# Performance work log

Measured on AMD Instinct MI355X. Metric: run time of the kernel, lower is better.

Reference implementation:

```python
import jax, jax.numpy as jnp
import numpy as np

M = 0.25      # margin m
GAMMA = 64.0  # scale gamma
N, D = 8192, 128
NUM_CLASSES = 512


def setup_inputs() -> dict:
    key = jax.random.key(0)
    k1, k2 = jax.random.split(key)
    inputs = jax.random.normal(k1, (N, D), dtype=jnp.float32)
    targets = jax.random.randint(k2, (N,), 0, NUM_CLASSES, dtype=jnp.int64)
    return {"inputs": inputs, "targets": targets}


def reference(inputs, targets):
    # L2-normalize rows -> cosine similarity matrix [n, n]
    x = inputs / jnp.linalg.norm(inputs, axis=1, keepdims=True)
    sim = x @ x.T
    # positive mask: same label (includes diagonal, matching the torch code)
    mask = targets[:, None] == targets[None, :]

    Op, On = 1.0 + M, -M
    delta_p, delta_n = 1.0 - M, M

    sim_d = jax.lax.stop_gradient(sim)  # .detach() in torch
    ap = jnp.maximum(Op - sim_d, 0.0)
    an = jnp.maximum(sim_d + On, 0.0)

    logit_p = -ap * (sim - delta_p) * GAMMA
    logit_n = an * (sim - delta_n) * GAMMA

    neg_inf = jnp.float32(-jnp.inf)
    # per-row logsumexp over positives of -logit_p, over negatives of logit_n
    lp = jax.nn.logsumexp(jnp.where(mask, -logit_p, neg_inf), axis=1)
    ln = jax.nn.logsumexp(jnp.where(mask, neg_inf, logit_n), axis=1)

    return jnp.mean(jax.nn.softplus(ln + lp))
```

## Files before the change

kernel.cpp:

```cpp
#include <hip/hip_runtime.h>
#include <math.h>


#define NR    8192
#define DIMK  128
#define NT    64
#define CHUNK 4
#define NBLKS 544

typedef __attribute__((ext_vector_type(8))) short short8;
typedef __attribute__((ext_vector_type(4))) float f32x4;
typedef __attribute__((address_space(3))) uint32_t lds_u32;
typedef const __attribute__((address_space(1))) uint32_t glb_u32;

__device__ __forceinline__ unsigned short bf16_rne(float f) {
  uint32_t u = __float_as_uint(f);
  u += 0x7FFFu + ((u >> 16) & 1u);
  return (unsigned short)(u >> 16);
}


__global__ __launch_bounds__(256) void normalize_split_kernel(
    const float* __restrict__ x, unsigned short* __restrict__ xhi,
    unsigned short* __restrict__ xlo, float* __restrict__ gP,
    float* __restrict__ gN, int* __restrict__ counter) {
  if (blockIdx.x < 32)      gP[blockIdx.x * 256 + threadIdx.x] = 0.f;
  else if (blockIdx.x < 64) gN[(blockIdx.x - 32) * 256 + threadIdx.x] = 0.f;
  if (blockIdx.x == 64 && threadIdx.x == 0) *counter = 0;

  const int wave = threadIdx.x >> 6;
  const int lane = threadIdx.x & 63;
  const int row  = blockIdx.x * 4 + wave;
  const float2 v = ((const float2*)(x + (size_t)row * DIMK))[lane];
  float ss = v.x * v.x + v.y * v.y;
  #pragma unroll
  for (int s = 1; s < 64; s <<= 1) ss += __shfl_xor(ss, s);
  const float r = rsqrtf(ss);
  const float a = v.x * r, b = v.y * r;
  const unsigned short ha = bf16_rne(a), hb = bf16_rne(b);
  const float haf = __uint_as_float((uint32_t)ha << 16);
  const float hbf = __uint_as_float((uint32_t)hb << 16);
  ushort2 hi, lo;
  hi.x = ha; hi.y = hb;
  lo.x = bf16_rne(a - haf); lo.y = bf16_rne(b - hbf);
  ((ushort2*)xhi)[(size_t)row * 64 + lane] = hi;
  ((ushort2*)xlo)[(size_t)row * 64 + lane] = lo;
}

__global__ __launch_bounds__(512, 2) void simloss_kernel(
    const unsigned short* __restrict__ xhi, const unsigned short* __restrict__ xlo,
    const int* __restrict__ tgt, float* __restrict__ gP, float* __restrict__ gN,
    int* __restrict__ counter, float* __restrict__ out) {
  __shared__ unsigned short S[32768];
  __shared__ int tAs[128];
  __shared__ int tBs[2][128];
  __shared__ float red[512];
  __shared__ int islast;

  const int tid  = threadIdx.x;
  const int wave = tid >> 6, lane = tid & 63;
  const int wy = wave & 3, wx = wave >> 2;
  const int q = lane >> 4, mcol = lane & 15;

  int w = blockIdx.x, bi = 0, sz = NT;
  while (w >= (sz + CHUNK - 1) / CHUNK) { w -= (sz + CHUNK - 1) / CHUNK; ++bi; --sz; }
  const int bj0 = bi + w * CHUNK;
  const int ntile = min(CHUNK, NT - bj0);
  const int i0 = bi * 128;

  {
    const unsigned short* ghA = xhi + (size_t)i0 * DIMK;
    const unsigned short* glA = xlo + (size_t)i0 * DIMK;
    #pragma unroll
    for (int g = 0; g < 4; ++g) {
      const int r  = wave * 16 + g * 4 + (lane >> 4);
      const int sc = (lane & 15) ^ (r & 15);
      __builtin_amdgcn_global_load_lds((glb_u32*)(ghA + (size_t)r * DIMK + sc * 8),
          (lds_u32*)&S[(wave * 16 + g * 4) * 128], 16, 0, 0);
      __builtin_amdgcn_global_load_lds((glb_u32*)(glA + (size_t)r * DIMK + sc * 8),
          (lds_u32*)&S[16384 + (wave * 16 + g * 4) * 128], 16, 0, 0);
    }
  }
  if (tid < 128) tAs[tid] = tgt[i0 + tid];
  __syncthreads();

  short8 Ah[2][4], Al[2][4];
  #pragma unroll
  for (int fr = 0; fr < 2; ++fr) {
    const int r = wy * 32 + fr * 16 + mcol;
    #pragma unroll
    for (int ks = 0; ks < 4; ++ks) {
      const int pc = (ks * 4 + q) ^ mcol;
      Ah[fr][ks] = *(const short8*)&S[r * 128 + pc * 8];
      Al[fr][ks] = *(const short8*)&S[16384 + r * 128 + pc * 8];
    }
  }
  int ta[2][4];
  #pragma unroll
  for (int fr = 0; fr < 2; ++fr)
    #pragma unroll
    for (int rg = 0; rg < 4; ++rg)
      ta[fr][rg] = tAs[wy * 32 + fr * 16 + q * 4 + rg];
  __builtin_amdgcn_s_waitcnt(0);
  __syncthreads();

  if (tid < 128) tBs[0][tid] = tgt[bj0 * 128 + tid];
  {
    const unsigned short* gb = xhi + (size_t)bj0 * 128 * DIMK;
    #pragma unroll
    for (int g = 0; g < 4; ++g) {
      const int r  = wave * 16 + g * 4 + (lane >> 4);
      const int sc = (lane & 15) ^ (r & 15);
      __builtin_amdgcn_global_load_lds((glb_u32*)(gb + (size_t)r * DIMK + sc * 8),
          (lds_u32*)&S[(wave * 16 + g * 4) * 128], 16, 0, 0);
    }
  }

  float rowP[2][4] = {{0.f}}, rowN[2][4] = {{0.f}};
  float pP[4], pN[4];
  int pcol = -1;

  for (int t = 0; t < ntile; ++t) {
    const int bj = bj0 + t;
    __builtin_amdgcn_s_waitcnt(112);
    __builtin_amdgcn_s_barrier();

    if (t + 1 < ntile) {
      if (tid < 128) tBs[(t + 1) & 1][tid] = tgt[(bj + 1) * 128 + tid];
      const unsigned short* gb = xhi + (size_t)(bj + 1) * 128 * DIMK;
      unsigned short* dst = &S[((t + 1) & 1) * 16384];
      #pragma unroll
      for (int g = 0; g < 4; ++g) {
        const int r  = wave * 16 + g * 4 + (lane >> 4);
        const int sc = (lane & 15) ^ (r & 15);
        __builtin_amdgcn_global_load_lds((glb_u32*)(gb + (size_t)r * DIMK + sc * 8),
            (lds_u32*)&dst[(wave * 16 + g * 4) * 128], 16, 0, 0);
      }
    }

    const unsigned short* Bb = &S[(t & 1) * 16384];
    f32x4 acc[2][4];
    #pragma unroll
    for (int fr = 0; fr < 2; ++fr)
      #pragma unroll
      for (int fc = 0; fc < 4; ++fc)
        acc[fr][fc] = (f32x4){0.f, 0.f, 0.f, 0.f};
    #pragma unroll
    for (int ks = 0; ks < 4; ++ks) {
      short8 bh[4];
      #pragma unroll
      for (int fc = 0; fc < 4; ++fc) {
        const int rb = wx * 64 + fc * 16 + mcol;
        const int pc = (ks * 4 + q) ^ mcol;
        bh[fc] = *(const short8*)&Bb[rb * 128 + pc * 8];
      }
      #pragma unroll
      for (int fc = 0; fc < 4; ++fc) {
        acc[0][fc] = __builtin_amdgcn_mfma_f32_16x16x32_bf16(Ah[0][ks], bh[fc], acc[0][fc], 0, 0, 0);
        acc[1][fc] = __builtin_amdgcn_mfma_f32_16x16x32_bf16(Ah[1][ks], bh[fc], acc[1][fc], 0, 0, 0);
        acc[0][fc] = __builtin_amdgcn_mfma_f32_16x16x32_bf16(Al[0][ks], bh[fc], acc[0][fc], 0, 0, 0);
        acc[1][fc] = __builtin_amdgcn_mfma_f32_16x16x32_bf16(Al[1][ks], bh[fc], acc[1][fc], 0, 0, 0);
      }
    }

    if (pcol >= 0) {
      #pragma unroll
      for (int fc = 0; fc < 4; ++fc) {
        float a = pP[fc], b = pN[fc];
        a += __shfl_xor(a, 16); a += __shfl_xor(a, 32);
        b += __shfl_xor(b, 16); b += __shfl_xor(b, 32);
        if (q == 0) {
          atomicAdd(&gP[pcol + fc * 16 + mcol], a);
          atomicAdd(&gN[pcol + fc * 16 + mcol], b);
        }
      }
    }

    int tb[4];
    #pragma unroll
    for (int fc = 0; fc < 4; ++fc) tb[fc] = tBs[t & 1][wx * 64 + fc * 16 + mcol];
    float cP[4] = {0.f, 0.f, 0.f, 0.f}, cN[4] = {0.f, 0.f, 0.f, 0.f};
    #pragma unroll
    for (int fr = 0; fr < 2; ++fr) {
      #pragma unroll
      for (int rg = 0; rg < 4; ++rg) {
        const int taa = ta[fr][rg];
        float vp = 0.f, vn = 0.f;
        #pragma unroll
        for (int fc = 0; fc < 4; ++fc) {
          const float s  = acc[fr][fc][rg];
          const bool pos = (taa == tb[fc]);
          const float ap = fmaxf(1.25f - s, 0.f);
          const float an = fmaxf(s - 0.25f, 0.f);
          const float arg = pos ? ap * fmaf(s, 64.f, -48.f) : an * an * 64.f;
          const float e = __expf(arg);
          const float ep = pos ? e : 0.f;
          const float en = pos ? 0.f : e;
          vp += ep; vn += en;
          cP[fc] += ep; cN[fc] += en;
        }
        rowP[fr][rg] += vp;
        rowN[fr][rg] += vn;
      }
    }
    if (bj != bi) {
      #pragma unroll
      for (int fc = 0; fc < 4; ++fc) { pP[fc] = cP[fc]; pN[fc] = cN[fc]; }
      pcol = bj * 128 + wx * 64;
    } else {
      pcol = -1;
    }
  }

  if (pcol >= 0) {
    #pragma unroll
    for (int fc = 0; fc < 4; ++fc) {
      float a = pP[fc], b = pN[fc];
      a += __shfl_xor(a, 16); a += __shfl_xor(a, 32);
      b += __shfl_xor(b, 16); b += __shfl_xor(b, 32);
      if (q == 0) {
        atomicAdd(&gP[pcol + fc * 16 + mcol], a);
        atomicAdd(&gN[pcol + fc * 16 + mcol], b);
      }
    }
  }

  #pragma unroll
  for (int fr = 0; fr < 2; ++fr) {
    #pragma unroll
    for (int rg = 0; rg < 4; ++rg) {
      float vp = rowP[fr][rg], vn = rowN[fr][rg];
      #pragma unroll
      for (int m = 1; m < 16; m <<= 1) {
        vp += __shfl_xor(vp, m);
        vn += __shfl_xor(vn, m);
      }
      if (mcol == 0) {
        const int row = i0 + wy * 32 + fr * 16 + q * 4 + rg;
        atomicAdd(&gP[row], vp);
        atomicAdd(&gN[row], vn);
      }
    }
  }

  __builtin_amdgcn_s_waitcnt(0);
  __syncthreads();
  if (tid == 0) islast = (atomicAdd(counter, 1) == NBLKS - 1) ? 1 : 0;
  __syncthreads();
  if (islast) {
    float local = 0.f;
    #pragma unroll 1
    for (int b = 0; b < 2; ++b) {
      const int base = b * 4096 + tid * 8;
      float p[8], n[8];
      #pragma unroll
      for (int u = 0; u < 8; ++u) p[u] = atomicAdd(&gP[base + u], 0.0f);
      #pragma unroll
      for (int u = 0; u < 8; ++u) n[u] = atomicAdd(&gN[base + u], 0.0f);
      #pragma unroll
      for (int u = 0; u < 8; ++u) local += log1pf(p[u] * n[u]);
    }
    red[tid] = local;
    __syncthreads();
    for (int s2 = 256; s2 > 0; s2 >>= 1) {
      if (tid < s2) red[tid] += red[tid + s2];
      __syncthreads();
    }
    if (tid == 0) out[0] = red[0] / (float)NR;
  }
}

extern "C" void kernel_launch(void* const* d_in, const int* in_sizes, int n_in,
                              void* d_out, int out_size, void* d_ws, size_t ws_size,
                              hipStream_t stream) {
  const float* x  = (const float*)d_in[0];
  const int* tgt  = (const int*)d_in[1];
  float* out      = (float*)d_out;

  unsigned short* xhi = (unsigned short*)d_ws;
  unsigned short* xlo = xhi + (size_t)NR * DIMK;
  float* gP = (float*)((char*)d_ws + (size_t)NR * DIMK * 4);
  float* gN = gP + NR;
  int* counter = (int*)(gN + NR);

  normalize_split_kernel<<<NR / 4, 256, 0, stream>>>(x, xhi, xlo, gP, gN, counter);
  simloss_kernel<<<NBLKS, 512, 0, stream>>>(xhi, xlo, tgt, gP, gN, counter, out);
}
```

Measured before the change: 130.8 us.

## Balance triangular tile work with paired row-strips and LDS column reduction

Replaces the chunked upper-triangle tile schedule (544 blocks with uneven tile counts) with a paired-strip scheme: strip p and strip 63-p are concatenated into 65 tiles split evenly across 16 blocks, so each of the 512 blocks gets 4-5 tiles. Column partial sums are now reduced across waves through an LDS buffer and written by a single wave, instead of every wave issuing atomics. B-tile staging is restricted to four of the waves, and the launch bound is raised to 4 blocks per CU. This adds extra barriers per tile and an A-strip reload at the strip switch, and the larger LDS footprint may keep the occupancy hint from being met.

```diff
diff --git a/kernel.cpp b/kernel.cpp
--- a/kernel.cpp
+++ b/kernel.cpp
@@ -5,8 +5,7 @@
 #define NR    8192
 #define DIMK  128
 #define NT    64
-#define CHUNK 4
-#define NBLKS 544
+#define NBLKS 512
 
 typedef __attribute__((ext_vector_type(8))) short short8;
 typedef __attribute__((ext_vector_type(4))) float f32x4;
@@ -47,13 +46,14 @@
   ((ushort2*)xlo)[(size_t)row * 64 + lane] = lo;
 }
 
-__global__ __launch_bounds__(512, 2) void simloss_kernel(
+__global__ __launch_bounds__(512, 4) void simloss_kernel(
     const unsigned short* __restrict__ xhi, const unsigned short* __restrict__ xlo,
     const int* __restrict__ tgt, float* __restrict__ gP, float* __restrict__ gN,
     int* __restrict__ counter, float* __restrict__ out) {
   __shared__ unsigned short S[32768];
-  __shared__ int tAs[128];
-  __shared__ int tBs[2][128];
+  __shared__ float colbuf[2][4][128][2];
+  __shared__ int tAs[2][128];
+  __shared__ int tBs[5][128];
   __shared__ float red[512];
   __shared__ int islast;
 
@@ -61,84 +61,132 @@
   const int wave = tid >> 6, lane = tid & 63;
   const int wy = wave & 3, wx = wave >> 2;
   const int q = lane >> 4, mcol = lane & 15;
-
-  int w = blockIdx.x, bi = 0, sz = NT;
-  while (w >= (sz + CHUNK - 1) / CHUNK) { w -= (sz + CHUNK - 1) / CHUNK; ++bi; --sz; }
-  const int bj0 = bi + w * CHUNK;
-  const int ntile = min(CHUNK, NT - bj0);
-  const int i0 = bi * 128;
-
-  {
-    const unsigned short* ghA = xhi + (size_t)i0 * DIMK;
-    const unsigned short* glA = xlo + (size_t)i0 * DIMK;
+  const bool isStage = (wy == 1) || (wy == 2);
+  const bool isFlush = (wy == 0);
+  const int srank = (wy - 1) + wx * 2;
+
+  const int p  = blockIdx.x >> 4;
+  const int b  = blockIdx.x & 15;
+  const int n1 = NT - p;
+  const int t0 = (b * (NT + 1)) >> 4;
+  const int t1 = ((b + 1) * (NT + 1)) >> 4;
+  const int ntile = t1 - t0;
+  const int p2 = NT - 1 - p;
+
+  int cur_bi = (t0 < n1) ? p : p2;
+
+  if (tid < 128)       tAs[0][tid] = tgt[cur_bi * 128 + tid];
+  else if (tid < 256)  tAs[1][tid - 128] = tgt[p2 * 128 + (tid - 128)];
+  for (int v = tid; v < ntile * 128; v += 512) {
+    const int ix = t0 + (v >> 7);
+    const int bj = (ix < n1) ? p + ix : p2 + (ix - n1);
+    tBs[v >> 7][v & 127] = tgt[bj * 128 + (v & 127)];
+  }
+
+  auto stageA = [&](int bi) {
+    const unsigned short* gh = xhi + (size_t)bi * 128 * DIMK;
+    const unsigned short* gl = xlo + (size_t)bi * 128 * DIMK;
     #pragma unroll
     for (int g = 0; g < 4; ++g) {
       const int r  = wave * 16 + g * 4 + (lane >> 4);
       const int sc = (lane & 15) ^ (r & 15);
-      __builtin_amdgcn_global_load_lds((glb_u32*)(ghA + (size_t)r * DIMK + sc * 8),
+      __builtin_amdgcn_global_load_lds((glb_u32*)(gh + (size_t)r * DIMK + sc * 8),
           (lds_u32*)&S[(wave * 16 + g * 4) * 128], 16, 0, 0);
-      __builtin_amdgcn_global_load_lds((glb_u32*)(glA + (size_t)r * DIMK + sc * 8),
+      __builtin_amdgcn_global_load_lds((glb_u32*)(gl + (size_t)r * DIMK + sc * 8),
           (lds_u32*)&S[16384 + (wave * 16 + g * 4) * 128], 16, 0, 0);
     }
-  }
-  if (tid < 128) tAs[tid] = tgt[i0 + tid];
-  __syncthreads();
-
-  short8 Ah[2][4], Al[2][4];
-  #pragma unroll
-  for (int fr = 0; fr < 2; ++fr) {
-    const int r = wy * 32 + fr * 16 + mcol;
-    #pragma unroll
-    for (int ks = 0; ks < 4; ++ks) {
-      const int pc = (ks * 4 + q) ^ mcol;
-      Ah[fr][ks] = *(const short8*)&S[r * 128 + pc * 8];
-      Al[fr][ks] = *(const short8*)&S[16384 + r * 128 + pc * 8];
-    }
-  }
-  int ta[2][4];
-  #pragma unroll
-  for (int fr = 0; fr < 2; ++fr)
-    #pragma unroll
-    for (int rg = 0; rg < 4; ++rg)
-      ta[fr][rg] = tAs[wy * 32 + fr * 16 + q * 4 + rg];
-  __builtin_amdgcn_s_waitcnt(0);
-  __syncthreads();
-
-  if (tid < 128) tBs[0][tid] = tgt[bj0 * 128 + tid];
-  {
-    const unsigned short* gb = xhi + (size_t)bj0 * 128 * DIMK;
-    #pragma unroll
-    for (int g = 0; g < 4; ++g) {
-      const int r  = wave * 16 + g * 4 + (lane >> 4);
+  };
+  auto stageB = [&](int bj, int buf) {
+    const unsigned short* gb = xhi + (size_t)bj * 128 * DIMK;
+    unsigned short* dst = &S[buf * 16384];
+    #pragma unroll
+    for (int g = 0; g < 8; ++g) {
+      const int r  = srank * 32 + g * 4 + (lane >> 4);
       const int sc = (lane & 15) ^ (r & 15);
       __builtin_amdgcn_global_load_lds((glb_u32*)(gb + (size_t)r * DIMK + sc * 8),
-          (lds_u32*)&S[(wave * 16 + g * 4) * 128], 16, 0, 0);
-    }
-  }
+          (lds_u32*)&dst[(srank * 32 + g * 4) * 128], 16, 0, 0);
+    }
+  };
+
+  short8 Ah[2][4], Al[2][4];
+  int ta[2][4];
+  auto extractA = [&](int seg) {
+    #pragma unroll
+    for (int fr = 0; fr < 2; ++fr) {
+      const int r = wy * 32 + fr * 16 + mcol;
+      #pragma unroll
+      for (int ks = 0; ks < 4; ++ks) {
+        const int pc = (ks * 4 + q) ^ mcol;
+        Ah[fr][ks] = *(const short8*)&S[r * 128 + pc * 8];
+        Al[fr][ks] = *(const short8*)&S[16384 + r * 128 + pc * 8];
+      }
+    }
+    #pragma unroll
+    for (int fr = 0; fr < 2; ++fr)
+      #pragma unroll
+      for (int rg = 0; rg < 4; ++rg)
+        ta[fr][rg] = tAs[seg][wy * 32 + fr * 16 + q * 4 + rg];
+  };
 
   float rowP[2][4] = {{0.f}}, rowN[2][4] = {{0.f}};
-  float pP[4], pN[4];
-  int pcol = -1;
-
-  for (int t = 0; t < ntile; ++t) {
-    const int bj = bj0 + t;
-    __builtin_amdgcn_s_waitcnt(112);
+  auto flushRows = [&](int bi) {
+    #pragma unroll
+    for (int fr = 0; fr < 2; ++fr)
+      #pragma unroll
+      for (int rg = 0; rg < 4; ++rg) {
+        float vp = rowP[fr][rg], vn = rowN[fr][rg];
+        #pragma unroll
+        for (int m = 1; m < 16; m <<= 1) {
+          vp += __shfl_xor(vp, m);
+          vn += __shfl_xor(vn, m);
+        }
+        if (mcol == 0) {
+          const int row = bi * 128 + wy * 32 + fr * 16 + q * 4 + rg;
+          atomicAdd(&gP[row], vp);
+          atomicAdd(&gN[row], vn);
+        }
+      }
+  };
+
+  stageA(cur_bi);
+  __syncthreads();
+  extractA(0);
+  __builtin_amdgcn_s_waitcnt(49279);
+  __builtin_amdgcn_s_barrier();
+  if (isStage) stageB((t0 < n1) ? p + t0 : p2 + (t0 - n1), 0);
+
+  for (int tl = 0; tl < ntile; ++tl) {
+    const int ix = t0 + tl;
+    const int bi = (ix < n1) ? p : p2;
+    const int bj = (ix < n1) ? p + ix : p2 + (ix - n1);
+
+    if (bi != cur_bi) {
+      flushRows(cur_bi);
+      cur_bi = bi;
+      stageA(cur_bi);
+      __syncthreads();
+      extractA(1);
+      #pragma unroll
+      for (int fr = 0; fr < 2; ++fr)
+        #pragma unroll
+        for (int rg = 0; rg < 4; ++rg) { rowP[fr][rg] = 0.f; rowN[fr][rg] = 0.f; }
+      __builtin_amdgcn_s_waitcnt(49279);
+      __builtin_amdgcn_s_barrier();
+      if (isStage) stageB(bj, tl & 1);
+    }
+
+    if (isStage) __builtin_amdgcn_s_waitcnt(112);
     __builtin_amdgcn_s_barrier();
 
-    if (t + 1 < ntile) {
-      if (tid < 128) tBs[(t + 1) & 1][tid] = tgt[(bj + 1) * 128 + tid];
-      const unsigned short* gb = xhi + (size_t)(bj + 1) * 128 * DIMK;
-      unsigned short* dst = &S[((t + 1) & 1) * 16384];
-      #pragma unroll
-      for (int g = 0; g < 4; ++g) {
-        const int r  = wave * 16 + g * 4 + (lane >> 4);
-        const int sc = (lane & 15) ^ (r & 15);
-        __builtin_amdgcn_global_load_lds((glb_u32*)(gb + (size_t)r * DIMK + sc * 8),
-            (lds_u32*)&dst[(wave * 16 + g * 4) * 128], 16, 0, 0);
-      }
-    }
-
-    const unsigned short* Bb = &S[(t & 1) * 16384];
+    if (tl + 1 < ntile) {
+      const int ix2 = ix + 1;
+      if ((ix2 < n1) == (ix < n1)) {
+        const int bj2 = (ix2 < n1) ? p + ix2 : p2 + (ix2 - n1);
+        if (isStage) stageB(bj2, (tl + 1) & 1);
+      }
+    }
+
+    const unsigned short* Bb = &S[(tl & 1) * 16384];
     f32x4 acc[2][4];
     #pragma unroll
     for (int fr = 0; fr < 2; ++fr)
@@ -163,22 +211,9 @@
       }
     }
 
-    if (pcol >= 0) {
-      #pragma unroll
-      for (int fc = 0; fc < 4; ++fc) {
-        float a = pP[fc], b = pN[fc];
-        a += __shfl_xor(a, 16); a += __shfl_xor(a, 32);
-        b += __shfl_xor(b, 16); b += __shfl_xor(b, 32);
-        if (q == 0) {
-          atomicAdd(&gP[pcol + fc * 16 + mcol], a);
-          atomicAdd(&gN[pcol + fc * 16 + mcol], b);
-        }
-      }
-    }
-
     int tb[4];
     #pragma unroll
-    for (int fc = 0; fc < 4; ++fc) tb[fc] = tBs[t & 1][wx * 64 + fc * 16 + mcol];
+    for (int fc = 0; fc < 4; ++fc) tb[fc] = tBs[tl][wx * 64 + fc * 16 + mcol];
     float cP[4] = {0.f, 0.f, 0.f, 0.f}, cN[4] = {0.f, 0.f, 0.f, 0.f};
     #pragma unroll
     for (int fr = 0; fr < 2; ++fr) {
@@ -203,45 +238,35 @@
         rowN[fr][rg] += vn;
       }
     }
-    if (bj != bi) {
-      #pragma unroll
-      for (int fc = 0; fc < 4; ++fc) { pP[fc] = cP[fc]; pN[fc] = cN[fc]; }
-      pcol = bj * 128 + wx * 64;
-    } else {
-      pcol = -1;
+
+    #pragma unroll
+    for (int fc = 0; fc < 4; ++fc) {
+      cP[fc] += __shfl_xor(cP[fc], 16); cP[fc] += __shfl_xor(cP[fc], 32);
+      cN[fc] += __shfl_xor(cN[fc], 16); cN[fc] += __shfl_xor(cN[fc], 32);
+    }
+    if (q == 0) {
+      #pragma unroll
+      for (int fc = 0; fc < 4; ++fc) {
+        float2 v; v.x = cP[fc]; v.y = cN[fc];
+        *(float2*)&colbuf[tl & 1][wy][wx * 64 + fc * 16 + mcol][0] = v;
+      }
+    }
+    __builtin_amdgcn_s_waitcnt(49279);
+    __builtin_amdgcn_s_barrier();
+
+    if (isFlush && bj != bi) {
+      const int col = wx * 64 + lane;
+      float sp = 0.f, sn = 0.f;
+      #pragma unroll
+      for (int w = 0; w < 4; ++w) {
+        const float2 v = *(const float2*)&colbuf[tl & 1][w][col][0];
+        sp += v.x; sn += v.y;
+      }
+      atomicAdd(&gP[bj * 128 + col], sp);
+      atomicAdd(&gN[bj * 128 + col], sn);
     }
   }
-
-  if (pcol >= 0) {
-    #pragma unroll
-    for (int fc = 0; fc < 4; ++fc) {
-      float a = pP[fc], b = pN[fc];
-      a += __shfl_xor(a, 16); a += __shfl_xor(a, 32);
-      b += __shfl_xor(b, 16); b += __shfl_xor(b, 32);
-      if (q == 0) {
-        atomicAdd(&gP[pcol + fc * 16 + mcol], a);
-        atomicAdd(&gN[pcol + fc * 16 + mcol], b);
-      }
-    }
-  }
-
-  #pragma unroll
-  for (int fr = 0; fr < 2; ++fr) {
-    #pragma unroll
-    for (int rg = 0; rg < 4; ++rg) {
-      float vp = rowP[fr][rg], vn = rowN[fr][rg];
-      #pragma unroll
-      for (int m = 1; m < 16; m <<= 1) {
-        vp += __shfl_xor(vp, m);
-        vn += __shfl_xor(vn, m);
-      }
-      if (mcol == 0) {
-        const int row = i0 + wy * 32 + fr * 16 + q * 4 + rg;
-        atomicAdd(&gP[row], vp);
-        atomicAdd(&gN[row], vn);
-      }
-    }
-  }
+  flushRows(cur_bi);
 
   __builtin_amdgcn_s_waitcnt(0);
   __syncthreads();
@@ -250,15 +275,15 @@
   if (islast) {
     float local = 0.f;
     #pragma unroll 1
-    for (int b = 0; b < 2; ++b) {
-      const int base = b * 4096 + tid * 8;
-      float p[8], n[8];
-      #pragma unroll
-      for (int u = 0; u < 8; ++u) p[u] = atomicAdd(&gP[base + u], 0.0f);
-      #pragma unroll
-      for (int u = 0; u < 8; ++u) n[u] = atomicAdd(&gN[base + u], 0.0f);
-      #pragma unroll
-      for (int u = 0; u < 8; ++u) local += log1pf(p[u] * n[u]);
+    for (int bb = 0; bb < 2; ++bb) {
+      const int base = bb * 4096 + tid * 8;
+      float pv[8], nv[8];
+      #pragma unroll
+      for (int u = 0; u < 8; ++u) pv[u] = atomicAdd(&gP[base + u], 0.0f);
+      #pragma unroll
+      for (int u = 0; u < 8; ++u) nv[u] = atomicAdd(&gN[base + u], 0.0f);
+      #pragma unroll
+      for (int u = 0; u < 8; ++u) local += log1pf(pv[u] * nv[u]);
     }
     red[tid] = local;
     __syncthreads();
```

Measured after the change: 182.6 us. +39.6%, slower.
